# Kernel optimization log

Hardware: AMD Instinct MI355X
Metric: run time of the kernel (lower is better)

Reference implementation:

```python
import jax, jax.numpy as jnp
import numpy as np
import itertools

# config: dim=256, resolution=14, key_dim=32, heads=8, attention_ratio=4, act=gelu (exact)
B, DIM, RES = 128, 256, 14
H, KD, DV = 8, 32, 128          # heads, key_dim, int(attention_ratio*key_dim)
N = RES * RES                    # 196 tokens
DH = H * DV                      # dim_head = 1024
SCALE = KD ** -0.5


def _bias_idxs():
    points = list(itertools.product(range(RES), range(RES)))
    offsets, idxs = {}, []
    for p1 in points:
        for p2 in points:
            off = (abs(p1[0] - p2[0]), abs(p1[1] - p2[1]))
            if off not in offsets:
                offsets[off] = len(offsets)
            idxs.append(offsets[off])
    return np.asarray(idxs, np.int32).reshape(N, N), len(offsets)


def _cbn(x, w, b, s, t):
    # 1x1 conv (as channel GEMM) + inference BatchNorm folded to per-channel affine
    y = jnp.einsum('bchw,co->bohw', x, w) + b[None, :, None, None]
    return y * s[None, :, None, None] + t[None, :, None, None]


def setup_inputs() -> dict:
    key = jax.random.key(0)
    ks = jax.random.split(key, 32)
    n = lambda i, sh, sc=0.05: jax.random.normal(ks[i], sh, jnp.float32) * sc
    idxs, noff = _bias_idxs()
    return {
        'hidden_states': jax.random.normal(ks[0], (B, DIM, RES, RES), jnp.float32),
        'w_q': n(1, (DIM, H * KD)), 'b_q': n(2, (H * KD,)), 's_q': 1.0 + n(3, (H * KD,)), 't_q': n(4, (H * KD,)),
        'w_k': n(5, (DIM, H * KD)), 'b_k': n(6, (H * KD,)), 's_k': 1.0 + n(7, (H * KD,)), 't_k': n(8, (H * KD,)),
        'w_v': n(9, (DIM, DH)), 'b_v': n(10, (DH,)), 's_v': 1.0 + n(11, (DH,)), 't_v': n(12, (DH,)),
        'w_vl': n(13, (DH, 1, 3, 3)), 'b_vl': n(14, (DH,)), 's_vl': 1.0 + n(15, (DH,)), 't_vl': n(16, (DH,)),
        'w_th1': n(17, (H, H), 0.2), 'b_th1': n(18, (H,)),
        'w_th2': n(19, (H, H), 0.2), 'b_th2': n(20, (H,)),
        'w_p': n(21, (DH, DIM)), 'b_p': n(22, (DIM,)), 's_p': 1.0 + n(23, (DIM,)), 't_p': n(24, (DIM,)),
        'attention_biases': n(25, (H, noff), 0.2),
        'bias_idxs': jnp.asarray(idxs),
    }


def reference(hidden_states, w_q, b_q, s_q, t_q, w_k, b_k, s_k, t_k,
              w_v, b_v, s_v, t_v, w_vl, b_vl, s_vl, t_vl,
              w_th1, b_th1, w_th2, b_th2, w_p, b_p, s_p, t_p,
              attention_biases, bias_idxs):
    b = hidden_states.shape[0]
    q = _cbn(hidden_states, w_q, b_q, s_q, t_q).reshape(b, H, KD, N).transpose(0, 1, 3, 2)  # [B,H,N,kd]
    k = _cbn(hidden_states, w_k, b_k, s_k, t_k).reshape(b, H, KD, N)                        # [B,H,kd,N]
    v_img = _cbn(hidden_states, w_v, b_v, s_v, t_v)                                          # [B,DH,res,res]
    vl = jax.lax.conv_general_dilated(v_img, w_vl, (1, 1), ((1, 1), (1, 1)),
                                      feature_group_count=DH,
                                      dimension_numbers=('NCHW', 'OIHW', 'NCHW'))
    vl = (vl + b_vl[None, :, None, None]) * s_vl[None, :, None, None] + t_vl[None, :, None, None]
    v = v_img.reshape(b, H, DV, N).transpose(0, 1, 3, 2)                                     # [B,H,N,dv]

    ab = attention_biases[:, bias_idxs]                                                      # [H,N,N]
    attn = jnp.einsum('bhnk,bhkm->bhnm', q, k) * SCALE + ab[None]                            # [B,H,N,N]
    attn = jnp.einsum('gh,bhnm->bgnm', w_th1, attn) + b_th1[None, :, None, None]             # talking head 1
    attn = jax.nn.softmax(attn, axis=-1)
    attn = jnp.einsum('gh,bhnm->bgnm', w_th2, attn) + b_th2[None, :, None, None]             # talking head 2

    out = jnp.einsum('bhnm,bhmd->bhnd', attn, v)                                             # [B,H,N,dv]
    out = out.transpose(0, 1, 3, 2).reshape(b, DH, RES, RES) + vl
    out = jax.nn.gelu(out, approximate=False)                                                # torch GELU (exact)
    return _cbn(out, w_p, b_p, s_p, t_p)                                                     # [B,dim,res,res]
```

## Files before the change

### kernel.cpp

```cpp
#include <hip/hip_runtime.h>
#include <hip/hip_bf16.h>

typedef __hip_bfloat16 bf16;
typedef __attribute__((ext_vector_type(8))) short bf16x8;
typedef __attribute__((ext_vector_type(8))) unsigned short u16x8;
typedef __attribute__((ext_vector_type(4))) float f32x4;

#define NB 128
#define CIN 256
#define NPIX 196
#define RESW 14
#define NH 8
#define KD 32
#define DV 128
#define DHID 1024
#define QKSCALE 0.17677669529663687f
#define QT 16
#define NTILE 13
#define VSTRIDE 224
#define ZPAD 232
#define XSP 264
#define GROWS 208

__device__ __forceinline__ float bf2f(unsigned short u) {
  union { unsigned int i; float f; } x; x.i = ((unsigned int)u) << 16; return x.f;
}
__device__ __forceinline__ unsigned short f2bfs(float f) {
  union { float f; unsigned int i; } u; u.f = f;
  unsigned int r = u.i + 0x7fffu + ((u.i >> 16) & 1u);
  return (unsigned short)(r >> 16);
}
__device__ __forceinline__ float gelu_exact(float x) {
  return x * 0.5f * (1.f + erff(x * 0.70710678118654752f));
}

__global__ void k_fold(
    const float* wq, const float* bq, const float* sq, const float* tq,
    const float* wk, const float* bk, const float* sk, const float* tk,
    const float* wv, const float* bv, const float* sv, const float* tv,
    const float* wvl, const float* bvl_in, const float* svl, const float* tvl,
    const float* wp, const float* bp_in, const float* sp, const float* tp,
    const float* abias, const int* bidx, const float* w1, const float* b1,
    int noff,
    short* Wt, short* Wpt, float* bcat, float* bpf, float* Wvl, float* bvlf,
    float* AB1)
{
  int i = blockIdx.x * 256 + threadIdx.x;
  if (i < 393216) {
    int o = i >> 8, c = i & 255;
    float w, s;
    if (o < 256)      { w = wq[c * 256 + o];          s = sq[o]; }
    else if (o < 512) { w = wk[c * 256 + (o - 256)];  s = sk[o - 256]; }
    else              { w = wv[c * 1024 + (o - 512)]; s = sv[o - 512]; }
    Wt[i] = (short)f2bfs(w * s);
    return;
  }
  i -= 393216;
  if (i < 1536) {
    float b, s, t;
    if (i < 256)      { b = bq[i];        s = sq[i];        t = tq[i]; }
    else if (i < 512) { b = bk[i - 256];  s = sk[i - 256];  t = tk[i - 256]; }
    else              { b = bv[i - 512];  s = sv[i - 512];  t = tv[i - 512]; }
    bcat[i] = b * s + t;
    return;
  }
  i -= 1536;
  if (i < 262144) {
    int o = i >> 10, ch = i & 1023;
    Wpt[i] = (short)f2bfs(wp[ch * 256 + o] * sp[o]);
    return;
  }
  i -= 262144;
  if (i < 256) { bpf[i] = bp_in[i] * sp[i] + tp[i]; return; }
  i -= 256;
  if (i < 9216) { int ch = i / 9; Wvl[i] = wvl[i] * svl[ch]; return; }
  i -= 9216;
  if (i < 1024) { bvlf[i] = bvl_in[i] * svl[i] + tvl[i]; return; }
  i -= 1024;
  if (i < NPIX * NPIX) {
    int idx = bidx[i];
    float a[8];
#pragma unroll
    for (int h = 0; h < 8; ++h) a[h] = abias[h * noff + idx];
#pragma unroll
    for (int g = 0; g < 8; ++g) {
      float z = b1[g];
#pragma unroll
      for (int h = 0; h < 8; ++h) z += w1[g * 8 + h] * a[h];
      AB1[(size_t)g * NPIX * NPIX + i] = z;
    }
    return;
  }
}

__global__ __launch_bounds__(512) void k_qkv(
    const float* __restrict__ X, const short* __restrict__ Wt,
    const float* __restrict__ bcat, bf16* __restrict__ Yq,
    bf16* __restrict__ Yk, bf16* __restrict__ Yv)
{
  __shared__ short Xs[112 * XSP];
  int b = blockIdx.x >> 1, half = blockIdx.x & 1;
  int t = threadIdx.x;
  const float* Xb = X + (size_t)b * CIN * NPIX;

  for (int i = t; i < 256 * 28; i += 512) {
    int c = i / 28, j = i % 28;
    int ng = half * 112 + 4 * j;
    int lr = 4 * j;
    if (ng + 3 < NPIX) {
      float4 xv = *(const float4*)(Xb + c * NPIX + ng);
      Xs[(lr + 0) * XSP + c] = (short)f2bfs(xv.x);
      Xs[(lr + 1) * XSP + c] = (short)f2bfs(xv.y);
      Xs[(lr + 2) * XSP + c] = (short)f2bfs(xv.z);
      Xs[(lr + 3) * XSP + c] = (short)f2bfs(xv.w);
    } else {
#pragma unroll
      for (int e = 0; e < 4; ++e) {
        float v = (ng + e < NPIX) ? Xb[c * NPIX + ng + e] : 0.f;
        Xs[(lr + e) * XSP + c] = (short)f2bfs(v);
      }
    }
  }
  __syncthreads();

  int w = t >> 6, lane = t & 63, nl = lane & 15, grp = lane >> 4;
  int NTH = half ? 6 : 7;
  int ntb = half * 7;

  for (int mm = w; mm < 192; mm += 8) {
    if (mm < 64) {
      int ot = mm >> 1, sub = mm & 1;
      int lt0 = sub * 4;
      int ltN = sub ? (NTH - 4) : 4;
      const short* arow = Wt + (size_t)(ot * 16 + nl) * CIN;
      f32x4 acc[4];
#pragma unroll
      for (int s = 0; s < 4; ++s) acc[s] = (f32x4){0.f, 0.f, 0.f, 0.f};
#pragma unroll
      for (int kk = 0; kk < 8; ++kk) {
        bf16x8 af = *(const bf16x8*)(arow + kk * 32 + grp * 8);
#pragma unroll
        for (int s = 0; s < 4; ++s) {
          if (s < ltN) {
            bf16x8 bfr = *(const bf16x8*)(Xs + ((lt0 + s) * 16 + nl) * XSP + kk * 32 + grp * 8);
            acc[s] = __builtin_amdgcn_mfma_f32_16x16x32_bf16(af, bfr, acc[s], 0, 0, 0);
          }
        }
      }
      int o0 = ot * 16 + grp * 4;
      float4 bb = *(const float4*)(bcat + o0);
      unsigned short* dst = (unsigned short*)((o0 < 256) ? Yq : Yk);
      int ob = o0 & 255;
#pragma unroll
      for (int s = 0; s < 4; ++s) {
        if (s < ltN) {
          int n = (ntb + lt0 + s) * 16 + nl;
          if (n < NPIX) {
            ushort4 pk;
            pk.x = f2bfs(acc[s][0] + bb.x); pk.y = f2bfs(acc[s][1] + bb.y);
            pk.z = f2bfs(acc[s][2] + bb.z); pk.w = f2bfs(acc[s][3] + bb.w);
            *(ushort4*)(dst + ((size_t)b * NPIX + n) * CIN + ob) = pk;
          }
        }
      }
    } else {
      int mm2 = mm - 64;
      int cht = mm2 >> 1, sub = mm2 & 1;
      int lt0 = sub * 4;
      int ltN = sub ? (NTH - 4) : 4;
      int ch = cht * 16 + nl;
      const short* brow = Wt + (size_t)(512 + ch) * CIN;
      f32x4 acc[4];
#pragma unroll
      for (int s = 0; s < 4; ++s) acc[s] = (f32x4){0.f, 0.f, 0.f, 0.f};
#pragma unroll
      for (int kk = 0; kk < 8; ++kk) {
        bf16x8 bfr = *(const bf16x8*)(brow + kk * 32 + grp * 8);
#pragma unroll
        for (int s = 0; s < 4; ++s) {
          if (s < ltN) {
            bf16x8 af = *(const bf16x8*)(Xs + ((lt0 + s) * 16 + nl) * XSP + kk * 32 + grp * 8);
            acc[s] = __builtin_amdgcn_mfma_f32_16x16x32_bf16(af, bfr, acc[s], 0, 0, 0);
          }
        }
      }
      float bb = bcat[512 + ch];
#pragma unroll
      for (int s = 0; s < 4; ++s) {
        if (s < ltN) {
          int m0 = (ntb + lt0 + s) * 16 + grp * 4;
          if (m0 + 3 < NPIX) {
            ushort4 pk;
            pk.x = f2bfs(acc[s][0] + bb); pk.y = f2bfs(acc[s][1] + bb);
            pk.z = f2bfs(acc[s][2] + bb); pk.w = f2bfs(acc[s][3] + bb);
            *(ushort4*)((unsigned short*)Yv + ((size_t)b * DHID + ch) * VSTRIDE + m0) = pk;
          }
        }
      }
    }
  }
}

__global__ __launch_bounds__(512) void k_conv(
    const bf16* __restrict__ Yv, const float* __restrict__ Wvl,
    const float* __restrict__ bvlf, bf16* __restrict__ Gt)
{
  __shared__ short Vs[128 * ZPAD];
  int b = blockIdx.x >> 3, cg = blockIdx.x & 7;
  int t = threadIdx.x;
  const unsigned short* src = (const unsigned short*)Yv + ((size_t)b * DHID + cg * 128) * VSTRIDE;
  for (int i = t; i < 128 * 28; i += 512) {
    int ch = i / 28, j = i % 28;
    u16x8 v = *(const u16x8*)(src + ch * VSTRIDE + j * 8);
    *(u16x8*)(Vs + ch * ZPAD + j * 8) = v;
  }
  __syncthreads();

  int ch = t & 127, yg = t >> 7;
  int chg = cg * 128 + ch;
  float w9[9];
#pragma unroll
  for (int k = 0; k < 9; ++k) w9[k] = Wvl[chg * 9 + k];
  float bb = bvlf[chg];
  const short* row = Vs + ch * ZPAD;
  unsigned short* gbase = (unsigned short*)Gt + (size_t)b * GROWS * DHID + chg;

  int ylim = (yg == 3) ? 2 : 4;
  for (int yy = 0; yy < ylim; ++yy) {
    int y = yg * 4 + yy;
    float rw[3][14];
#pragma unroll
    for (int dy = 0; dy < 3; ++dy) {
      int ys = y + dy - 1;
      if (ys < 0 || ys >= RESW) {
#pragma unroll
        for (int x = 0; x < 14; ++x) rw[dy][x] = 0.f;
      } else {
#pragma unroll
        for (int x2 = 0; x2 < 7; ++x2) {
          unsigned int u = *(const unsigned int*)(row + ys * RESW + x2 * 2);
          rw[dy][x2 * 2]     = bf2f((unsigned short)(u & 0xffffu));
          rw[dy][x2 * 2 + 1] = bf2f((unsigned short)(u >> 16));
        }
      }
    }
#pragma unroll
    for (int x = 0; x < 14; ++x) {
      float a = bb;
#pragma unroll
      for (int dy = 0; dy < 3; ++dy)
#pragma unroll
        for (int dx = 0; dx < 3; ++dx) {
          int xx = x + dx - 1;
          if (xx >= 0 && xx < RESW) a += w9[dy * 3 + dx] * rw[dy][xx];
        }
      gbase[(size_t)(y * RESW + x) * DHID] = f2bfs(a);
    }
  }
}

__global__ __launch_bounds__(512) void k_attn(
    const bf16* __restrict__ Yq, const bf16* __restrict__ Yk,
    const bf16* __restrict__ Yv, const float* __restrict__ AB1,
    const float* __restrict__ w1, const float* __restrict__ w2,
    const float* __restrict__ b2, bf16* __restrict__ Gt)
{
  __shared__ short zb[NH][QT][ZPAD];
  __shared__ float red[8][NH][16];
  int id = blockIdx.x;
  int swz = (id & 7) * (NB * NTILE / 8) + (id >> 3);
  int b = swz / NTILE, tile = swz % NTILE;
  int n0 = tile * QT;
  int t = threadIdx.x;
  int w = t >> 6, lane = t & 63;
  int nl = lane & 15, grp = lane >> 4;
  int n = n0 + nl;
  int nA = (n < NPIX) ? n : (NPIX - 1);

  int t0 = w;
  int t1 = (w < 5) ? (w + 8) : ((w == 5) ? 13 : -1);

  const short* qrow = (const short*)Yq + ((size_t)b * NPIX + nA) * CIN;
  bf16x8 qf[8];
#pragma unroll
  for (int h = 0; h < 8; ++h) qf[h] = *(const bf16x8*)(qrow + h * 32 + grp * 8);

  const short* kbase = (const short*)Yk + (size_t)b * NPIX * CIN;
  const f32x4 NEG = (f32x4){-1e30f, -1e30f, -1e30f, -1e30f};
  f32x4 zm0[8], zm1[8];

#define DO_TILE(MT, ZM)                                                        \
  {                                                                            \
    int m0_ = (MT) * 16 + grp * 4;                                             \
    bool mv_ = (m0_ + 3) < NPIX;                                               \
    if ((MT) < 13) {                                                           \
      int mrow_ = (MT) * 16 + nl; if (mrow_ > NPIX - 1) mrow_ = NPIX - 1;      \
      const short* krow_ = kbase + (size_t)mrow_ * CIN + grp * 8;              \
      f32x4 zr_[8];                                                            \
      _Pragma("unroll")                                                        \
      for (int h = 0; h < 8; ++h) {                                            \
        bf16x8 kf_ = *(const bf16x8*)(krow_ + h * 32);                         \
        zr_[h] = __builtin_amdgcn_mfma_f32_16x16x32_bf16(                      \
            kf_, qf[h], (f32x4){0.f, 0.f, 0.f, 0.f}, 0, 0, 0);                 \
      }                                                                        \
      _Pragma("unroll")                                                        \
      for (int g = 0; g < 8; ++g) {                                            \
        if (mv_) {                                                             \
          f32x4 a_ = *(const f32x4*)(AB1 + ((size_t)g * NPIX + nA) * NPIX + m0_); \
          _Pragma("unroll")                                                    \
          for (int h = 0; h < 8; ++h) {                                        \
            float wgh_ = w1[g * 8 + h] * QKSCALE;                              \
            _Pragma("unroll")                                                  \
            for (int r = 0; r < 4; ++r) a_[r] += wgh_ * zr_[h][r];             \
          }                                                                    \
          ZM[g] = a_;                                                          \
        } else ZM[g] = NEG;                                                    \
      }                                                                        \
    } else {                                                                   \
      _Pragma("unroll")                                                        \
      for (int g = 0; g < 8; ++g) ZM[g] = NEG;                                 \
    }                                                                          \
  }

  DO_TILE(t0, zm0)
  if (t1 >= 0) { DO_TILE(t1, zm1) }
  else {
#pragma unroll
    for (int g = 0; g < 8; ++g) zm1[g] = NEG;
  }

  float mg[8];
#pragma unroll
  for (int g = 0; g < 8; ++g) {
    float m_ = fmaxf(fmaxf(zm0[g][0], zm0[g][1]), fmaxf(zm0[g][2], zm0[g][3]));
    m_ = fmaxf(m_, fmaxf(fmaxf(zm1[g][0], zm1[g][1]), fmaxf(zm1[g][2], zm1[g][3])));
    m_ = fmaxf(m_, __shfl_xor(m_, 16));
    m_ = fmaxf(m_, __shfl_xor(m_, 32));
    mg[g] = m_;
  }
  if (lane < 16) {
#pragma unroll
    for (int g = 0; g < 8; ++g) red[w][g][nl] = mg[g];
  }
  __syncthreads();
  float fmx[8];
#pragma unroll
  for (int g = 0; g < 8; ++g) {
    float m_ = red[0][g][nl];
#pragma unroll
    for (int ww = 1; ww < 8; ++ww) m_ = fmaxf(m_, red[ww][g][nl]);
    fmx[g] = m_;
  }
  float sg[8];
#pragma unroll
  for (int g = 0; g < 8; ++g) {
    float s_ = 0.f;
#pragma unroll
    for (int r = 0; r < 4; ++r) { zm0[g][r] = __expf(zm0[g][r] - fmx[g]); s_ += zm0[g][r]; }
#pragma unroll
    for (int r = 0; r < 4; ++r) { zm1[g][r] = __expf(zm1[g][r] - fmx[g]); s_ += zm1[g][r]; }
    s_ += __shfl_xor(s_, 16);
    s_ += __shfl_xor(s_, 32);
    sg[g] = s_;
  }
  __syncthreads();
  if (lane < 16) {
#pragma unroll
    for (int g = 0; g < 8; ++g) red[w][g][nl] = sg[g];
  }
  __syncthreads();
  float inv[8];
#pragma unroll
  for (int g = 0; g < 8; ++g) {
    float s_ = red[0][g][nl];
#pragma unroll
    for (int ww = 1; ww < 8; ++ww) s_ += red[ww][g][nl];
    inv[g] = 1.f / s_;
  }

#define WR_TILE(MT, ZM)                                                        \
  {                                                                            \
    int m0_ = (MT) * 16 + grp * 4;                                             \
    _Pragma("unroll")                                                          \
    for (int g = 0; g < 8; ++g) {                                              \
      ushort4 pk_;                                                             \
      pk_.x = f2bfs(ZM[g][0] * inv[g]); pk_.y = f2bfs(ZM[g][1] * inv[g]);      \
      pk_.z = f2bfs(ZM[g][2] * inv[g]); pk_.w = f2bfs(ZM[g][3] * inv[g]);      \
      *(ushort4*)&zb[g][nl][m0_] = pk_;                                        \
    }                                                                          \
  }
  WR_TILE(t0, zm0)
  if (t1 >= 0) WR_TILE(t1, zm1)

  unsigned short* gp = (unsigned short*)Gt + ((size_t)b * GROWS + nA) * DHID + w * DV;
  ushort4 cvv[8];
#pragma unroll
  for (int dt = 0; dt < 8; ++dt) cvv[dt] = *(const ushort4*)(gp + dt * 16 + grp * 4);
  __syncthreads();

  float w2r[8];
#pragma unroll
  for (int h = 0; h < 8; ++h) w2r[h] = w2[w * 8 + h];
  float b2j = b2[w];
  f32x4 accO[8];
#pragma unroll
  for (int dt = 0; dt < 8; ++dt) accO[dt] = (f32x4){0.f, 0.f, 0.f, 0.f};
  const short* vbase = (const short*)Yv + ((size_t)b * DHID + w * DV) * VSTRIDE;
#pragma unroll
  for (int ks = 0; ks < 7; ++ks) {
    int moff = ks * 32 + grp * 8;
    bf16x8 rd[8];
#pragma unroll
    for (int gg = 0; gg < 8; ++gg) rd[gg] = *(const bf16x8*)&zb[gg][nl][moff];
    bf16x8 Bf;
#pragma unroll
    for (int jj = 0; jj < 8; ++jj) {
      int m = moff + jj;
      float a = (m < NPIX) ? b2j : 0.f;
#pragma unroll
      for (int gg = 0; gg < 8; ++gg) a += w2r[gg] * bf2f((unsigned short)rd[gg][jj]);
      Bf[jj] = (short)f2bfs(a);
    }
#pragma unroll
    for (int dt = 0; dt < 8; ++dt) {
      bf16x8 Af = *(const bf16x8*)(vbase + (size_t)(dt * 16 + nl) * VSTRIDE + moff);
      accO[dt] = __builtin_amdgcn_mfma_f32_16x16x32_bf16(Af, Bf, accO[dt], 0, 0, 0);
    }
  }

  if (n < NPIX) {
#pragma unroll
    for (int dt = 0; dt < 8; ++dt) {
      ushort4 pk;
      float pre;
      pre = accO[dt][0] + bf2f(cvv[dt].x); pk.x = f2bfs(gelu_exact(pre));
      pre = accO[dt][1] + bf2f(cvv[dt].y); pk.y = f2bfs(gelu_exact(pre));
      pre = accO[dt][2] + bf2f(cvv[dt].z); pk.z = f2bfs(gelu_exact(pre));
      pre = accO[dt][3] + bf2f(cvv[dt].w); pk.w = f2bfs(gelu_exact(pre));
      *(ushort4*)(gp + dt * 16 + grp * 4) = pk;
    }
  }
}

__global__ __launch_bounds__(256) void k_proj(
    const bf16* __restrict__ Gt, const short* __restrict__ Wpt,
    const float* __restrict__ bpf, float* __restrict__ out)
{
  int b = blockIdx.x >> 1, half = blockIdx.x & 1;
  int t = threadIdx.x, w = t >> 6, lane = t & 63, nl = lane & 15, grp = lane >> 4;
  int ot0 = half * 8 + w;
  int ot1 = ot0 + 4;
  const short* a0 = Wpt + (size_t)(ot0 * 16 + nl) * DHID + grp * 8;
  const short* a1 = Wpt + (size_t)(ot1 * 16 + nl) * DHID + grp * 8;
  const short* bb = (const short*)Gt + (size_t)b * GROWS * DHID + (size_t)nl * DHID + grp * 8;
  f32x4 acc0[13], acc1[13];
#pragma unroll
  for (int i = 0; i < 13; ++i) {
    acc0[i] = (f32x4){0.f, 0.f, 0.f, 0.f};
    acc1[i] = (f32x4){0.f, 0.f, 0.f, 0.f};
  }
  for (int kk = 0; kk < 32; ++kk) {
    bf16x8 af0 = *(const bf16x8*)(a0 + kk * 32);
    bf16x8 af1 = *(const bf16x8*)(a1 + kk * 32);
#pragma unroll
    for (int nt = 0; nt < 13; ++nt) {
      bf16x8 bfr = *(const bf16x8*)(bb + (size_t)(nt * 16) * DHID + kk * 32);
      acc0[nt] = __builtin_amdgcn_mfma_f32_16x16x32_bf16(af0, bfr, acc0[nt], 0, 0, 0);
      acc1[nt] = __builtin_amdgcn_mfma_f32_16x16x32_bf16(af1, bfr, acc1[nt], 0, 0, 0);
    }
  }
  int o0 = ot0 * 16 + grp * 4;
  int o1 = ot1 * 16 + grp * 4;
  float4 b0 = *(const float4*)(bpf + o0);
  float4 b1v = *(const float4*)(bpf + o1);
  float b0a[4] = {b0.x, b0.y, b0.z, b0.w};
  float b1a[4] = {b1v.x, b1v.y, b1v.z, b1v.w};
#pragma unroll
  for (int nt = 0; nt < 13; ++nt) {
    int nn = nt * 16 + nl;
    if (nn < NPIX) {
#pragma unroll
      for (int r = 0; r < 4; ++r) {
        out[((size_t)b * CIN + o0 + r) * NPIX + nn] = acc0[nt][r] + b0a[r];
        out[((size_t)b * CIN + o1 + r) * NPIX + nn] = acc1[nt][r] + b1a[r];
      }
    }
  }
}

extern "C" void kernel_launch(void* const* d_in, const int* in_sizes, int n_in,
                              void* d_out, int out_size, void* d_ws, size_t ws_size,
                              hipStream_t stream) {
  const float* X    = (const float*)d_in[0];
  const float* wq   = (const float*)d_in[1];
  const float* bq   = (const float*)d_in[2];
  const float* sq   = (const float*)d_in[3];
  const float* tq   = (const float*)d_in[4];
  const float* wk   = (const float*)d_in[5];
  const float* bk   = (const float*)d_in[6];
  const float* sk   = (const float*)d_in[7];
  const float* tk   = (const float*)d_in[8];
  const float* wv   = (const float*)d_in[9];
  const float* bv   = (const float*)d_in[10];
  const float* sv   = (const float*)d_in[11];
  const float* tv   = (const float*)d_in[12];
  const float* wvl  = (const float*)d_in[13];
  const float* bvl  = (const float*)d_in[14];
  const float* svl  = (const float*)d_in[15];
  const float* tvl  = (const float*)d_in[16];
  const float* w1   = (const float*)d_in[17];
  const float* b1   = (const float*)d_in[18];
  const float* w2   = (const float*)d_in[19];
  const float* b2   = (const float*)d_in[20];
  const float* wp   = (const float*)d_in[21];
  const float* bpp  = (const float*)d_in[22];
  const float* sp   = (const float*)d_in[23];
  const float* tp   = (const float*)d_in[24];
  const float* ab   = (const float*)d_in[25];
  const int*   bidx = (const int*)d_in[26];
  int noff = in_sizes[25] / NH;

  short* Wt   = (short*)d_ws;
  short* Wpt  = Wt + 393216;
  float* bcat = (float*)(Wpt + 262144);
  float* bpf  = bcat + 1536;
  float* Wvl  = bpf + 256;
  float* bvlf = Wvl + 9216;
  float* AB1  = bvlf + 1024;
  short* Yq   = (short*)(AB1 + 307328);
  short* Yk   = Yq + (size_t)NB * NPIX * CIN;
  short* Yv   = Yk + (size_t)NB * NPIX * CIN;
  short* Gt   = Yv + (size_t)NB * DHID * VSTRIDE;

  k_fold<<<2758, 256, 0, stream>>>(wq, bq, sq, tq, wk, bk, sk, tk,
                                   wv, bv, sv, tv, wvl, bvl, svl, tvl,
                                   wp, bpp, sp, tp, ab, bidx, w1, b1, noff,
                                   Wt, Wpt, bcat, bpf, Wvl, bvlf, AB1);
  k_qkv<<<NB * 2, 512, 0, stream>>>(X, Wt, bcat, (bf16*)Yq, (bf16*)Yk, (bf16*)Yv);
  k_conv<<<NB * 8, 512, 0, stream>>>((const bf16*)Yv, Wvl, bvlf, (bf16*)Gt);
  k_attn<<<NB * NTILE, 512, 0, stream>>>((const bf16*)Yq, (const bf16*)Yk,
                                         (const bf16*)Yv, AB1, w1, w2, b2, (bf16*)Gt);
  k_proj<<<NB * 2, 256, 0, stream>>>((const bf16*)Gt, Wpt, bpf, (float*)d_out);
}
```

Measured before the change: 483.7 us.

## Split qkv/proj grids across more blocks and mix talking-head-2 before LDS

k_qkv and k_proj now launch four blocks per batch instead of two. Each block covers half the output tiles in k_qkv, and one output-tile group per wave in k_proj, which raises occupancy on the many CUs. In k_attn the second talking-head mixing moves from the PV inner loop, where every wave recomputed it from all heads, to a single pass in fp32 registers before the LDS write. Each wave then just loads its own head's probabilities. This cuts redundant ALU and LDS reads, at the cost of reloading X tiles more often in qkv and more register pressure in attn.

```diff
diff --git a/kernel.cpp b/kernel.cpp
--- a/kernel.cpp
+++ b/kernel.cpp
@@ -99,7 +99,7 @@
     bf16* __restrict__ Yk, bf16* __restrict__ Yv)
 {
   __shared__ short Xs[112 * XSP];
-  int b = blockIdx.x >> 1, half = blockIdx.x & 1;
+  int b = blockIdx.x >> 2, half = (blockIdx.x >> 1) & 1, og = blockIdx.x & 1;
   int t = threadIdx.x;
   const float* Xb = X + (size_t)b * CIN * NPIX;
 
@@ -127,7 +127,7 @@
   int NTH = half ? 6 : 7;
   int ntb = half * 7;
 
-  for (int mm = w; mm < 192; mm += 8) {
+  for (int mm = og * 96 + w; mm < og * 96 + 96; mm += 8) {
     if (mm < 64) {
       int ot = mm >> 1, sub = mm & 1;
       int lt0 = sub * 4;
@@ -279,6 +279,11 @@
 
   int t0 = w;
   int t1 = (w < 5) ? (w + 8) : ((w == 5) ? 13 : -1);
+
+  unsigned short* gp = (unsigned short*)Gt + ((size_t)b * GROWS + nA) * DHID + w * DV;
+  ushort4 cvv[8];
+#pragma unroll
+  for (int dt = 0; dt < 8; ++dt) cvv[dt] = *(const ushort4*)(gp + dt * 16 + grp * 4);
 
   const short* qrow = (const short*)Yq + ((size_t)b * NPIX + nA) * CIN;
   bf16x8 qf[8];
@@ -378,30 +383,45 @@
     inv[g] = 1.f / s_;
   }
 
-#define WR_TILE(MT, ZM)                                                        \
-  {                                                                            \
-    int m0_ = (MT) * 16 + grp * 4;                                             \
-    _Pragma("unroll")                                                          \
-    for (int g = 0; g < 8; ++g) {                                              \
-      ushort4 pk_;                                                             \
-      pk_.x = f2bfs(ZM[g][0] * inv[g]); pk_.y = f2bfs(ZM[g][1] * inv[g]);      \
-      pk_.z = f2bfs(ZM[g][2] * inv[g]); pk_.w = f2bfs(ZM[g][3] * inv[g]);      \
-      *(ushort4*)&zb[g][nl][m0_] = pk_;                                        \
-    }                                                                          \
-  }
-  WR_TILE(t0, zm0)
-  if (t1 >= 0) WR_TILE(t1, zm1)
-
-  unsigned short* gp = (unsigned short*)Gt + ((size_t)b * GROWS + nA) * DHID + w * DV;
-  ushort4 cvv[8];
-#pragma unroll
-  for (int dt = 0; dt < 8; ++dt) cvv[dt] = *(const ushort4*)(gp + dt * 16 + grp * 4);
+  float p0[8][4], p1[8][4];
+#pragma unroll
+  for (int g = 0; g < 8; ++g)
+#pragma unroll
+    for (int r = 0; r < 4; ++r) {
+      p0[g][r] = zm0[g][r] * inv[g];
+      p1[g][r] = zm1[g][r] * inv[g];
+    }
+  int m0a = t0 * 16 + grp * 4;
+  bool v0 = m0a < NPIX;
+  int m0b = (t1 >= 0) ? (t1 * 16 + grp * 4) : 0;
+  bool v1 = (t1 >= 0) && (m0b < NPIX);
+#pragma unroll
+  for (int j = 0; j < 8; ++j) {
+    float b2j = b2[j];
+    float a0[4] = {b2j, b2j, b2j, b2j};
+    float a1[4] = {b2j, b2j, b2j, b2j};
+#pragma unroll
+    for (int g = 0; g < 8; ++g) {
+      float wv = w2[j * 8 + g];
+#pragma unroll
+      for (int r = 0; r < 4; ++r) {
+        a0[r] += wv * p0[g][r];
+        a1[r] += wv * p1[g][r];
+      }
+    }
+    ushort4 pk0;
+    if (v0) { pk0.x = f2bfs(a0[0]); pk0.y = f2bfs(a0[1]); pk0.z = f2bfs(a0[2]); pk0.w = f2bfs(a0[3]); }
+    else    { pk0.x = 0; pk0.y = 0; pk0.z = 0; pk0.w = 0; }
+    *(ushort4*)&zb[j][nl][m0a] = pk0;
+    if (t1 >= 0) {
+      ushort4 pk1;
+      if (v1) { pk1.x = f2bfs(a1[0]); pk1.y = f2bfs(a1[1]); pk1.z = f2bfs(a1[2]); pk1.w = f2bfs(a1[3]); }
+      else    { pk1.x = 0; pk1.y = 0; pk1.z = 0; pk1.w = 0; }
+      *(ushort4*)&zb[j][nl][m0b] = pk1;
+    }
+  }
   __syncthreads();
 
-  float w2r[8];
-#pragma unroll
-  for (int h = 0; h < 8; ++h) w2r[h] = w2[w * 8 + h];
-  float b2j = b2[w];
   f32x4 accO[8];
 #pragma unroll
   for (int dt = 0; dt < 8; ++dt) accO[dt] = (f32x4){0.f, 0.f, 0.f, 0.f};
@@ -409,18 +429,7 @@
 #pragma unroll
   for (int ks = 0; ks < 7; ++ks) {
     int moff = ks * 32 + grp * 8;
-    bf16x8 rd[8];
-#pragma unroll
-    for (int gg = 0; gg < 8; ++gg) rd[gg] = *(const bf16x8*)&zb[gg][nl][moff];
-    bf16x8 Bf;
-#pragma unroll
-    for (int jj = 0; jj < 8; ++jj) {
-      int m = moff + jj;
-      float a = (m < NPIX) ? b2j : 0.f;
-#pragma unroll
-      for (int gg = 0; gg < 8; ++gg) a += w2r[gg] * bf2f((unsigned short)rd[gg][jj]);
-      Bf[jj] = (short)f2bfs(a);
-    }
+    bf16x8 Bf = *(const bf16x8*)&zb[w][nl][moff];
 #pragma unroll
     for (int dt = 0; dt < 8; ++dt) {
       bf16x8 Af = *(const bf16x8*)(vbase + (size_t)(dt * 16 + nl) * VSTRIDE + moff);
@@ -446,44 +455,32 @@
     const bf16* __restrict__ Gt, const short* __restrict__ Wpt,
     const float* __restrict__ bpf, float* __restrict__ out)
 {
-  int b = blockIdx.x >> 1, half = blockIdx.x & 1;
+  int b = blockIdx.x >> 2, q = blockIdx.x & 3;
   int t = threadIdx.x, w = t >> 6, lane = t & 63, nl = lane & 15, grp = lane >> 4;
-  int ot0 = half * 8 + w;
-  int ot1 = ot0 + 4;
-  const short* a0 = Wpt + (size_t)(ot0 * 16 + nl) * DHID + grp * 8;
-  const short* a1 = Wpt + (size_t)(ot1 * 16 + nl) * DHID + grp * 8;
+  int ot = q * 4 + w;
+  const short* a0 = Wpt + (size_t)(ot * 16 + nl) * DHID + grp * 8;
   const short* bb = (const short*)Gt + (size_t)b * GROWS * DHID + (size_t)nl * DHID + grp * 8;
-  f32x4 acc0[13], acc1[13];
-#pragma unroll
-  for (int i = 0; i < 13; ++i) {
-    acc0[i] = (f32x4){0.f, 0.f, 0.f, 0.f};
-    acc1[i] = (f32x4){0.f, 0.f, 0.f, 0.f};
-  }
+  f32x4 acc[13];
+#pragma unroll
+  for (int i = 0; i < 13; ++i) acc[i] = (f32x4){0.f, 0.f, 0.f, 0.f};
   for (int kk = 0; kk < 32; ++kk) {
-    bf16x8 af0 = *(const bf16x8*)(a0 + kk * 32);
-    bf16x8 af1 = *(const bf16x8*)(a1 + kk * 32);
+    bf16x8 af = *(const bf16x8*)(a0 + kk * 32);
 #pragma unroll
     for (int nt = 0; nt < 13; ++nt) {
       bf16x8 bfr = *(const bf16x8*)(bb + (size_t)(nt * 16) * DHID + kk * 32);
-      acc0[nt] = __builtin_amdgcn_mfma_f32_16x16x32_bf16(af0, bfr, acc0[nt], 0, 0, 0);
-      acc1[nt] = __builtin_amdgcn_mfma_f32_16x16x32_bf16(af1, bfr, acc1[nt], 0, 0, 0);
-    }
-  }
-  int o0 = ot0 * 16 + grp * 4;
-  int o1 = ot1 * 16 + grp * 4;
-  float4 b0 = *(const float4*)(bpf + o0);
-  float4 b1v = *(const float4*)(bpf + o1);
-  float b0a[4] = {b0.x, b0.y, b0.z, b0.w};
-  float b1a[4] = {b1v.x, b1v.y, b1v.z, b1v.w};
+      acc[nt] = __builtin_amdgcn_mfma_f32_16x16x32_bf16(af, bfr, acc[nt], 0, 0, 0);
+    }
+  }
+  int o0 = ot * 16 + grp * 4;
+  float4 bv = *(const float4*)(bpf + o0);
+  float ba[4] = {bv.x, bv.y, bv.z, bv.w};
 #pragma unroll
   for (int nt = 0; nt < 13; ++nt) {
     int nn = nt * 16 + nl;
     if (nn < NPIX) {
 #pragma unroll
-      for (int r = 0; r < 4; ++r) {
-        out[((size_t)b * CIN + o0 + r) * NPIX + nn] = acc0[nt][r] + b0a[r];
-        out[((size_t)b * CIN + o1 + r) * NPIX + nn] = acc1[nt][r] + b1a[r];
-      }
+      for (int r = 0; r < 4; ++r)
+        out[((size_t)b * CIN + o0 + r) * NPIX + nn] = acc[nt][r] + ba[r];
     }
   }
 }
@@ -536,9 +533,9 @@
                                    wv, bv, sv, tv, wvl, bvl, svl, tvl,
                                    wp, bpp, sp, tp, ab, bidx, w1, b1, noff,
                                    Wt, Wpt, bcat, bpf, Wvl, bvlf, AB1);
-  k_qkv<<<NB * 2, 512, 0, stream>>>(X, Wt, bcat, (bf16*)Yq, (bf16*)Yk, (bf16*)Yv);
+  k_qkv<<<NB * 4, 512, 0, stream>>>(X, Wt, bcat, (bf16*)Yq, (bf16*)Yk, (bf16*)Yv);
   k_conv<<<NB * 8, 512, 0, stream>>>((const bf16*)Yv, Wvl, bvlf, (bf16*)Gt);
   k_attn<<<NB * NTILE, 512, 0, stream>>>((const bf16*)Yq, (const bf16*)Yk,
                                          (const bf16*)Yv, AB1, w1, w2, b2, (bf16*)Gt);
-  k_proj<<<NB * 2, 256, 0, stream>>>((const bf16*)Gt, Wpt, bpf, (float*)d_out);
-}
+  k_proj<<<NB * 4, 256, 0, stream>>>((const bf16*)Gt, Wpt, bpf, (float*)d_out);
+}
```

Result: slower. 525.2 us (+8.6%).
